# Kernel tuning notes

Hardware: AMD Instinct MI355X
Metric: run time of the kernel (lower is better)

Reference implementation:

```python
import jax, jax.numpy as jnp
import numpy as np

L = 15      # GNN layers
D = 128     # hidden width


def _mlp3(x, w1, b1, w2, b2, w3, b3):
    h = jax.nn.relu(x @ w1 + b1)
    h = jax.nn.relu(h @ w2 + b2)
    return h @ w3 + b3


def _layernorm(x, g, b, eps=1e-5):
    mu = x.mean(-1, keepdims=True)
    var = ((x - mu) ** 2).mean(-1, keepdims=True)
    return (x - mu) / jnp.sqrt(var + eps) * g + b


def _gather(V, idx):
    # V: [B,N,D], idx: [B,E] -> [B,E,D]
    return jax.vmap(lambda v, i: v[i])(V, idx)


def _scatter_sum(e, idx, n):
    # e: [B,E,D], idx: [B,E] -> [B,n,D]
    return jax.vmap(lambda ee, ii: jnp.zeros((n, ee.shape[-1]), ee.dtype).at[ii].add(ee))(e, idx)


def setup_inputs() -> dict:
    key = jax.random.key(0)
    ks = iter(jax.random.split(key, 64))
    B, N, Eg = 1, 10000, 40000

    def lin(fi, fo, pre=()):
        s = 1.0 / np.sqrt(fi)
        w = jax.random.uniform(next(ks), pre + (fi, fo), jnp.float32, -s, s)
        b = jax.random.uniform(next(ks), pre + (fo,), jnp.float32, -s, s)
        return w, b

    inp = {}
    inp['node_pos'] = jax.random.normal(next(ks), (B, N, 3), jnp.float32)
    inp['areas'] = jax.random.uniform(next(ks), (B, N, 1), jnp.float32)
    inp['info'] = jax.random.normal(next(ks), (B, 1, 8), jnp.float32)
    inp['edges'] = jax.random.randint(next(ks), (B, Eg, 2), 0, N, jnp.int32)

    # Encoder MLPs (layer_norm=True)
    for pre, fi in [('fv', 12), ('fe', 4)]:
        w1, b1 = lin(fi, D); w2, b2 = lin(D, D); w3, b3 = lin(D, D)
        inp[pre + '_w1'], inp[pre + '_b1'] = w1, b1
        inp[pre + '_w2'], inp[pre + '_b2'] = w2, b2
        inp[pre + '_w3'], inp[pre + '_b3'] = w3, b3
        inp[pre + '_g'] = jnp.ones((D,), jnp.float32)
        inp[pre + '_bt'] = jnp.zeros((D,), jnp.float32)

    # 15 GNN layers, stacked along leading axis (layer_norm=False)
    for pre, fi in [('ge', D + 2 * D), ('gn', D + D)]:
        w1, b1 = lin(fi, D, (L,)); w2, b2 = lin(D, D, (L,)); w3, b3 = lin(D, D, (L,))
        inp[pre + '_w1'], inp[pre + '_b1'] = w1, b1
        inp[pre + '_w2'], inp[pre + '_b2'] = w2, b2
        inp[pre + '_w3'], inp[pre + '_b3'] = w3, b3

    # Decoder (layer_norm=False, output_size=1)
    w1, b1 = lin(D, D); w2, b2 = lin(D, D); w3, b3 = lin(D, 1)
    inp['de_w1'], inp['de_b1'] = w1, b1
    inp['de_w2'], inp['de_b2'] = w2, b2
    inp['de_w3'], inp['de_b3'] = w3, b3
    return inp


def reference(node_pos, areas, info, edges,
              fv_w1, fv_b1, fv_w2, fv_b2, fv_w3, fv_b3, fv_g, fv_bt,
              fe_w1, fe_b1, fe_w2, fe_b2, fe_w3, fe_b3, fe_g, fe_bt,
              ge_w1, ge_b1, ge_w2, ge_b2, ge_w3, ge_b3,
              gn_w1, gn_b1, gn_w2, gn_b2, gn_w3, gn_b3,
              de_w1, de_b1, de_w2, de_b2, de_w3, de_b3):
    B, N, _ = node_pos.shape
    info_b = jnp.broadcast_to(info, (B, N, info.shape[-1]))
    en_in = jnp.concatenate([node_pos, areas, info_b], -1)  # [B,N,12]

    s, r = edges[..., 0], edges[..., 1]
    dist = _gather(node_pos, s) - _gather(node_pos, r)      # [B,E,3]
    nrm = jnp.sqrt((dist ** 2).sum(-1, keepdims=True))
    E_raw = jnp.concatenate([dist, nrm], -1)                # [B,E,4]

    V = _layernorm(_mlp3(en_in, fv_w1, fv_b1, fv_w2, fv_b2, fv_w3, fv_b3), fv_g, fv_bt)
    E = _layernorm(_mlp3(E_raw, fe_w1, fe_b1, fe_w2, fe_b2, fe_w3, fe_b3), fe_g, fe_bt)

    def step(carry, p):
        V, E = carry
        w1, b1, w2, b2, w3, b3, nw1, nb1, nw2, nb2, nw3, nb3 = p
        e_in = jnp.concatenate([_gather(V, s), _gather(V, r), E], -1)  # [B,E,384]
        e_emb = _mlp3(e_in, w1, b1, w2, b2, w3, b3)
        agg = _scatter_sum(e_emb, s, N)                                # [B,N,128]
        v_emb = _mlp3(jnp.concatenate([V, agg], -1), nw1, nb1, nw2, nb2, nw3, nb3)
        return (V + v_emb, E + e_emb), None

    (V, E), _ = jax.lax.scan(step, (V, E),
                             (ge_w1, ge_b1, ge_w2, ge_b2, ge_w3, ge_b3,
                              gn_w1, gn_b1, gn_w2, gn_b2, gn_w3, gn_b3))

    return _mlp3(V, de_w1, de_b1, de_w2, de_b2, de_w3, de_b3)  # [B,N,1]
```

## Files before the change

kernel.cpp:

```cpp
#include <hip/hip_runtime.h>

#define DD 128
#define N_NODE 10000
#define N_EDGE 40000
#define N_LAYER 15

typedef unsigned short U16;
typedef __attribute__((ext_vector_type(8))) short short8;
typedef __attribute__((ext_vector_type(4))) float f32x4;

enum { A_BF16 = 0, A_EDGE, A_NODE, A_ENCIN, A_ERAW };
enum { EPI_F = 0, EPI_EDGE, EPI_NODE, EPI_DEC };

#define OFF_FV1 0
#define OFF_FV2 4096
#define OFF_FV3 20480
#define OFF_FE1 36864
#define OFF_FE2 40960
#define OFF_FE3 57344
#define OFF_GE1 73728
#define OFF_GE2 811008
#define OFF_GE3 1056768
#define OFF_GN1 1302528
#define OFF_GN2 1794048
#define OFF_GN3 2039808
#define OFF_DE1 2285568
#define OFF_DE2 2301952
#define WT_TOTAL 2318336

static __device__ __forceinline__ U16 f2b(float f) {
    union { float f; unsigned u; } x; x.f = f;
    unsigned u = x.u;
    return (U16)((u + 0x7fffu + ((u >> 16) & 1u)) >> 16);
}
static __device__ __forceinline__ float b2f(U16 u) {
    union { unsigned u; float f; } x; x.u = ((unsigned)u) << 16;
    return x.f;
}

static __device__ __forceinline__ void wgb() {
    __asm__ __volatile__("s_waitcnt lgkmcnt(0)\n\ts_barrier" ::: "memory");
}

struct I4x2 { int4 a, b; };

__global__ __launch_bounds__(256)
void wprep(const float* fv1, const float* fv2, const float* fv3,
           const float* fe1, const float* fe2, const float* fe3,
           const float* ge1, const float* ge2, const float* ge3,
           const float* gn1, const float* gn2, const float* gn3,
           const float* de1, const float* de2, U16* Wt)
{
    int b = blockIdx.x;
    const float* src; U16* dst; int K, Kpad, k0;
    if      (b < 1)   { src = fv1; K = 12;  Kpad = 32;  dst = Wt + OFF_FV1; k0 = b * 32; }
    else if (b < 5)   { src = fv2; K = 128; Kpad = 128; dst = Wt + OFF_FV2; k0 = (b-1)*32; }
    else if (b < 9)   { src = fv3; K = 128; Kpad = 128; dst = Wt + OFF_FV3; k0 = (b-5)*32; }
    else if (b < 10)  { src = fe1; K = 4;   Kpad = 32;  dst = Wt + OFF_FE1; k0 = (b-9)*32; }
    else if (b < 14)  { src = fe2; K = 128; Kpad = 128; dst = Wt + OFF_FE2; k0 = (b-10)*32; }
    else if (b < 18)  { src = fe3; K = 128; Kpad = 128; dst = Wt + OFF_FE3; k0 = (b-14)*32; }
    else if (b < 198) { int r = b-18,  mi = r/12, s = r%12; src = ge1 + (size_t)mi*384*128; K = 384; Kpad = 384; dst = Wt + OFF_GE1 + (size_t)mi*49152; k0 = s*32; }
    else if (b < 258) { int r = b-198, mi = r/4,  s = r%4;  src = ge2 + (size_t)mi*16384;   K = 128; Kpad = 128; dst = Wt + OFF_GE2 + (size_t)mi*16384; k0 = s*32; }
    else if (b < 318) { int r = b-258, mi = r/4,  s = r%4;  src = ge3 + (size_t)mi*16384;   K = 128; Kpad = 128; dst = Wt + OFF_GE3 + (size_t)mi*16384; k0 = s*32; }
    else if (b < 438) { int r = b-318, mi = r/8,  s = r%8;  src = gn1 + (size_t)mi*32768;   K = 256; Kpad = 256; dst = Wt + OFF_GN1 + (size_t)mi*32768; k0 = s*32; }
    else if (b < 498) { int r = b-438, mi = r/4,  s = r%4;  src = gn2 + (size_t)mi*16384;   K = 128; Kpad = 128; dst = Wt + OFF_GN2 + (size_t)mi*16384; k0 = s*32; }
    else if (b < 558) { int r = b-498, mi = r/4,  s = r%4;  src = gn3 + (size_t)mi*16384;   K = 128; Kpad = 128; dst = Wt + OFF_GN3 + (size_t)mi*16384; k0 = s*32; }
    else if (b < 562) { src = de1; K = 128; Kpad = 128; dst = Wt + OFF_DE1; k0 = (b-558)*32; }
    else              { src = de2; K = 128; Kpad = 128; dst = Wt + OFF_DE2; k0 = (b-562)*32; }

    __shared__ float T[32][129];
    #pragma unroll
    for (int i = 0; i < 16; ++i) {
        int l = threadIdx.x + i * 256;
        int kk = l >> 7, n = l & 127;
        int kg = k0 + kk;
        T[kk][n] = (kg < K) ? src[(size_t)kg * 128 + n] : 0.f;
    }
    __syncthreads();
    int n = threadIdx.x >> 1, h = threadIdx.x & 1;
    union { U16 u[16]; int4 v[2]; } o;
    #pragma unroll
    for (int j = 0; j < 16; ++j) o.u[j] = f2b(T[h * 16 + j][n]);
    int4* d = (int4*)(dst + (size_t)n * Kpad + k0 + h * 16);
    d[0] = o.v[0]; d[1] = o.v[1];
}

__global__ __launch_bounds__(256)
void csr_hist(const int* __restrict__ edges, int* __restrict__ cnt, int Eg)
{
    int e = blockIdx.x * 256 + threadIdx.x;
    if (e < Eg) atomicAdd(&cnt[edges[2 * e]], 1);
}

__global__ __launch_bounds__(256)
void csr_scan(const int* __restrict__ cnt, int* __restrict__ rowptr,
              int* __restrict__ cursor, int n)
{
    __shared__ int ps[256];
    int t = threadIdx.x, base = t * 40;
    int s = 0;
    for (int j = 0; j < 40; ++j) if (base + j < n) s += cnt[base + j];
    ps[t] = s; __syncthreads();
    for (int off = 1; off < 256; off <<= 1) {
        int v = (t >= off) ? ps[t - off] : 0;
        __syncthreads();
        ps[t] += v;
        __syncthreads();
    }
    int run = ps[t] - s;
    for (int j = 0; j < 40; ++j) {
        if (base + j < n) {
            rowptr[base + j] = run;
            cursor[base + j] = run;
            run += cnt[base + j];
        }
    }
    if (t == 255) rowptr[n] = ps[255];
}

__global__ __launch_bounds__(256)
void csr_scatter(const int* __restrict__ edges, int* __restrict__ cursor,
                 int* __restrict__ spos, int Eg)
{
    int e = blockIdx.x * 256 + threadIdx.x;
    if (e < Eg) spos[e] = atomicAdd(&cursor[edges[2 * e]], 1);
}

template<int ASRC, int EPI, int K1>
__global__ __launch_bounds__(256)
void mlp3(const U16* __restrict__ Af,
          const U16* __restrict__ W1, const float* __restrict__ b1,
          const U16* __restrict__ W2, const float* __restrict__ b2,
          const U16* __restrict__ W3, const float* __restrict__ b3,
          U16* __restrict__ outh, float* __restrict__ outf,
          const int* __restrict__ edges, const int* __restrict__ rowptr,
          const int* __restrict__ spos, float* __restrict__ eEs,
          const U16* __restrict__ Vh, const U16* __restrict__ Ehp,
          const float* __restrict__ pos, const float* __restrict__ area,
          const float* __restrict__ info, const float* __restrict__ w3f,
          int M)
{
    __shared__ U16 As[2][64][40];
    __shared__ U16 Bs[2][128][40];
    __shared__ U16 Hs[64][132];

    const int tid  = threadIdx.x;
    const int row0 = blockIdx.x * 64;
    const int wave = tid >> 6, lane = tid & 63;
    const int quad = lane >> 4, l16 = lane & 15;
    const int wm = (wave >> 1) * 32;
    const int wn = (wave & 1) * 64;
    const int sr = tid >> 2, sh = tid & 3;
    const int br = tid >> 1, bh = tid & 1;
    const int sm = row0 + sr;
    const bool valid = (sm < M);

    int si = 0, ri = 0, jbeg = 0, jend = 0;
    if ((ASRC == A_EDGE || ASRC == A_ERAW) && valid) {
        si = edges[2 * sm]; ri = edges[2 * sm + 1];
    }
    if (ASRC == A_NODE && valid) { jbeg = rowptr[sm]; jend = rowptr[sm + 1]; }

    f32x4 acc[4][2];

    auto zacc = [&] {
        #pragma unroll
        for (int i = 0; i < 4; ++i)
            #pragma unroll
            for (int j = 0; j < 2; ++j) acc[i][j] = (f32x4)0.f;
    };

    auto ldA = [&](int c) -> int4 {
        if (ASRC == A_ENCIN || ASRC == A_ERAW) {
            union { U16 u[8]; int4 v; } pk;
            #pragma unroll
            for (int j = 0; j < 8; ++j) pk.u[j] = 0;
            if (valid) {
                if (ASRC == A_ENCIN) {
                    #pragma unroll
                    for (int j = 0; j < 8; ++j) {
                        int col = sh * 8 + j;
                        float x = 0.f;
                        if (col < 3)       x = pos[3 * sm + col];
                        else if (col == 3) x = area[sm];
                        else if (col < 12) x = info[col - 4];
                        pk.u[j] = f2b(x);
                    }
                } else if (sh == 0) {
                    float dx = pos[3*si]   - pos[3*ri];
                    float dy = pos[3*si+1] - pos[3*ri+1];
                    float dz = pos[3*si+2] - pos[3*ri+2];
                    float nm = sqrtf(dx*dx + dy*dy + dz*dz);
                    pk.u[0] = f2b(dx); pk.u[1] = f2b(dy);
                    pk.u[2] = f2b(dz); pk.u[3] = f2b(nm);
                }
            }
            return pk.v;
        } else if (ASRC == A_NODE && c >= 4) {
            float a[8];
            #pragma unroll
            for (int i = 0; i < 8; ++i) a[i] = 0.f;
            if (valid) {
                const float* base = eEs + (c - 4) * 32 + sh * 8;
                for (int j = jbeg; j < jend; ++j) {
                    const float4* r = (const float4*)(base + (size_t)j * 128);
                    float4 x0 = r[0], x1 = r[1];
                    a[0]+=x0.x; a[1]+=x0.y; a[2]+=x0.z; a[3]+=x0.w;
                    a[4]+=x1.x; a[5]+=x1.y; a[6]+=x1.z; a[7]+=x1.w;
                }
            }
            union { U16 u[8]; int4 v; } pk;
            #pragma unroll
            for (int i = 0; i < 8; ++i) pk.u[i] = f2b(a[i]);
            return pk.v;
        } else {
            const U16* s;
            if (ASRC == A_BF16)        s = Af + (size_t)sm * K1 + c * 32;
            else if (ASRC == A_EDGE) {
                if (c < 4)             s = Vh  + (size_t)si * 128 + c * 32;
                else if (c < 8)        s = Vh  + (size_t)ri * 128 + (c - 4) * 32;
                else                   s = Ehp + (size_t)sm * 128 + (c - 8) * 32;
            } else                     s = Vh  + (size_t)sm * 128 + c * 32;
            return valid ? *(const int4*)(s + sh * 8) : make_int4(0,0,0,0);
        }
    };

    auto ldW = [&](const U16* W, int Kw, int c) -> I4x2 {
        const U16* s = W + (size_t)br * Kw + c * 32 + bh * 16;
        I4x2 r;
        r.a = ((const int4*)s)[0];
        r.b = ((const int4*)s)[1];
        return r;
    };

    auto wrA = [&](int b, int4 v) { *(int4*)&As[b][sr][sh * 8] = v; };
    auto wrW = [&](int b, I4x2 w) {
        *(int4*)&Bs[b][br][bh * 16]     = w.a;
        *(int4*)&Bs[b][br][bh * 16 + 8] = w.b;
    };

    auto mfA = [&](int b) {
        short8 wf[4], af[2];
        #pragma unroll
        for (int g = 0; g < 4; ++g)
            wf[g] = *(const short8*)&Bs[b][wn + g*16 + l16][quad * 8];
        #pragma unroll
        for (int g = 0; g < 2; ++g)
            af[g] = *(const short8*)&As[b][wm + g*16 + l16][quad * 8];
        #pragma unroll
        for (int wg = 0; wg < 4; ++wg)
            #pragma unroll
            for (int ag = 0; ag < 2; ++ag)
                acc[wg][ag] = __builtin_amdgcn_mfma_f32_16x16x32_bf16(
                    wf[wg], af[ag], acc[wg][ag], 0, 0, 0);
    };

    auto mfH = [&](int c, int b) {
        short8 wf[4], af[2];
        #pragma unroll
        for (int g = 0; g < 4; ++g)
            wf[g] = *(const short8*)&Bs[b][wn + g*16 + l16][quad * 8];
        #pragma unroll
        for (int g = 0; g < 2; ++g)
            af[g] = *(const short8*)&Hs[wm + g*16 + l16][c * 32 + quad * 8];
        #pragma unroll
        for (int wg = 0; wg < 4; ++wg)
            #pragma unroll
            for (int ag = 0; ag < 2; ++ag)
                acc[wg][ag] = __builtin_amdgcn_mfma_f32_16x16x32_bf16(
                    wf[wg], af[ag], acc[wg][ag], 0, 0, 0);
    };

    auto hwrite = [&](const float* bias) {
        #pragma unroll
        for (int wg = 0; wg < 4; ++wg) {
            f32x4 bv = *(const f32x4*)&bias[wn + wg*16 + quad*4];
            #pragma unroll
            for (int ag = 0; ag < 2; ++ag) {
                int m  = wm + ag*16 + l16;
                int n0 = wn + wg*16 + quad*4;
                union { U16 u[4]; uint2 q; } pk;
                #pragma unroll
                for (int rg = 0; rg < 4; ++rg)
                    pk.u[rg] = f2b(fmaxf(acc[wg][ag][rg] + bv[rg], 0.f));
                *(uint2*)&Hs[m][n0] = pk.q;
            }
        }
    };

    int4 ra0, ra1; I4x2 rw0, rw1;
    constexpr int C1 = K1 / 32;

    zacc();
    ra0 = ldA(0); rw0 = ldW(W1, K1, 0);
    if (C1 > 1) { ra1 = ldA(1); rw1 = ldW(W1, K1, 1); }
    wrA(0, ra0); wrW(0, rw0);
    wgb();
    #pragma unroll
    for (int c = 0; c < C1; ++c) {
        if (c + 2 < C1) {
            if ((c & 1) == 0) { ra0 = ldA(c + 2); rw0 = ldW(W1, K1, c + 2); }
            else              { ra1 = ldA(c + 2); rw1 = ldW(W1, K1, c + 2); }
        }
        if (c + 1 < C1) {
            if (((c + 1) & 1) == 0) { wrA(0, ra0); wrW(0, rw0); }
            else                    { wrA(1, ra1); wrW(1, rw1); }
        }
        mfA(c & 1);
        wgb();
    }

    rw0 = ldW(W2, 128, 0); rw1 = ldW(W2, 128, 1);
    hwrite(b1);
    wgb();
    zacc();
    wrW(0, rw0);
    wgb();
    #pragma unroll
    for (int c = 0; c < 4; ++c) {
        if (c + 2 < 4) {
            if ((c & 1) == 0) rw0 = ldW(W2, 128, c + 2);
            else              rw1 = ldW(W2, 128, c + 2);
        }
        if (c + 1 < 4) {
            if (((c + 1) & 1) == 0) wrW(0, rw0);
            else                    wrW(1, rw1);
        }
        mfH(c, c & 1);
        wgb();
    }

    if (EPI == EPI_DEC) {
        hwrite(b2);
        wgb();
        int mg = row0 + sr;
        float v = 0.f;
        if (mg < M) {
            const U16* hr = &Hs[sr][sh * 32];
            const float* wr = w3f + sh * 32;
            #pragma unroll
            for (int j = 0; j < 32; ++j) v += b2f(hr[j]) * wr[j];
        }
        v += __shfl_xor(v, 1);
        v += __shfl_xor(v, 2);
        if (sh == 0 && mg < M) outf[mg] = v + b3[0];
        return;
    }

    rw0 = ldW(W3, 128, 0); rw1 = ldW(W3, 128, 1);
    hwrite(b2);
    wgb();
    zacc();
    wrW(0, rw0);
    wgb();
    #pragma unroll
    for (int c = 0; c < 4; ++c) {
        if (c + 2 < 4) {
            if ((c & 1) == 0) rw0 = ldW(W3, 128, c + 2);
            else              rw1 = ldW(W3, 128, c + 2);
        }
        if (c + 1 < 4) {
            if (((c + 1) & 1) == 0) wrW(0, rw0);
            else                    wrW(1, rw1);
        }
        mfH(c, c & 1);
        wgb();
    }

    f32x4 bvs[4];
    #pragma unroll
    for (int wg = 0; wg < 4; ++wg)
        bvs[wg] = *(const f32x4*)&b3[wn + wg*16 + quad*4];
    #pragma unroll
    for (int ag = 0; ag < 2; ++ag) {
        int mg = row0 + wm + ag*16 + l16;
        if (mg >= M) continue;
        int sp = 0;
        if (EPI == EPI_EDGE) sp = spos[mg];
        #pragma unroll
        for (int wg = 0; wg < 4; ++wg) {
            int n0 = wn + wg*16 + quad*4;
            f32x4 v;
            #pragma unroll
            for (int rg = 0; rg < 4; ++rg) v[rg] = acc[wg][ag][rg] + bvs[wg][rg];
            size_t o = (size_t)mg * 128 + n0;
            if (EPI == EPI_F) {
                *(f32x4*)&outf[o] = v;
            } else {
                f32x4 c = *(f32x4*)&outf[o];
                c += v;
                *(f32x4*)&outf[o] = c;
                union { U16 u[4]; uint2 q; } pk;
                #pragma unroll
                for (int rg = 0; rg < 4; ++rg) pk.u[rg] = f2b(c[rg]);
                *(uint2*)&outh[o] = pk.q;
                if (EPI == EPI_EDGE)
                    *(f32x4*)&eEs[(size_t)sp * 128 + n0] = v;
            }
        }
    }
}

__global__ __launch_bounds__(256)
void ln_kernel(float* __restrict__ X, const float* __restrict__ g,
               const float* __restrict__ b, U16* __restrict__ Xh, int rows)
{
    int row  = blockIdx.x * 4 + (threadIdx.x >> 6);
    int lane = threadIdx.x & 63;
    if (row >= rows) return;
    float x0 = X[row * DD + lane];
    float x1 = X[row * DD + 64 + lane];
    float s = x0 + x1, q = x0 * x0 + x1 * x1;
    #pragma unroll
    for (int off = 32; off; off >>= 1) {
        s += __shfl_xor(s, off);
        q += __shfl_xor(q, off);
    }
    float mu  = s * (1.f / 128.f);
    float var = q * (1.f / 128.f) - mu * mu;
    float inv = rsqrtf(var + 1e-5f);
    float y0 = (x0 - mu) * inv * g[lane]      + b[lane];
    float y1 = (x1 - mu) * inv * g[64 + lane] + b[64 + lane];
    X[row * DD + lane]       = y0;
    X[row * DD + 64 + lane]  = y1;
    Xh[row * DD + lane]      = f2b(y0);
    Xh[row * DD + 64 + lane] = f2b(y1);
}

extern "C" void kernel_launch(void* const* d_in, const int* in_sizes, int n_in,
                              void* d_out, int out_size, void* d_ws, size_t ws_size,
                              hipStream_t stream)
{
    (void)in_sizes; (void)n_in; (void)out_size; (void)ws_size;

    const float* pos   = (const float*)d_in[0];
    const float* area  = (const float*)d_in[1];
    const float* info  = (const float*)d_in[2];
    const int*   edges = (const int*)d_in[3];
    const float* fv_w1 = (const float*)d_in[4];
    const float* fv_b1 = (const float*)d_in[5];
    const float* fv_w2 = (const float*)d_in[6];
    const float* fv_b2 = (const float*)d_in[7];
    const float* fv_w3 = (const float*)d_in[8];
    const float* fv_b3 = (const float*)d_in[9];
    const float* fv_g  = (const float*)d_in[10];
    const float* fv_bt = (const float*)d_in[11];
    const float* fe_w1 = (const float*)d_in[12];
    const float* fe_b1 = (const float*)d_in[13];
    const float* fe_w2 = (const float*)d_in[14];
    const float* fe_b2 = (const float*)d_in[15];
    const float* fe_w3 = (const float*)d_in[16];
    const float* fe_b3 = (const float*)d_in[17];
    const float* fe_g  = (const float*)d_in[18];
    const float* fe_bt = (const float*)d_in[19];
    const float* ge_w1 = (const float*)d_in[20];
    const float* ge_b1 = (const float*)d_in[21];
    const float* ge_w2 = (const float*)d_in[22];
    const float* ge_b2 = (const float*)d_in[23];
    const float* ge_w3 = (const float*)d_in[24];
    const float* ge_b3 = (const float*)d_in[25];
    const float* gn_w1 = (const float*)d_in[26];
    const float* gn_b1 = (const float*)d_in[27];
    const float* gn_w2 = (const float*)d_in[28];
    const float* gn_b2 = (const float*)d_in[29];
    const float* gn_w3 = (const float*)d_in[30];
    const float* gn_b3 = (const float*)d_in[31];
    const float* de_w1 = (const float*)d_in[32];
    const float* de_b1 = (const float*)d_in[33];
    const float* de_w2 = (const float*)d_in[34];
    const float* de_b2 = (const float*)d_in[35];
    const float* de_w3 = (const float*)d_in[36];
    const float* de_b3 = (const float*)d_in[37];

    char* p = (char*)d_ws;
    float* Vf   = (float*)p;  p += (size_t)N_NODE * 128 * 4;
    float* Ef   = (float*)p;  p += (size_t)N_EDGE * 128 * 4;
    float* eEs  = (float*)p;  p += (size_t)N_EDGE * 128 * 4;
    U16*  Vh    = (U16*)p;    p += (size_t)N_NODE * 128 * 2;
    U16*  Eh    = (U16*)p;    p += (size_t)N_EDGE * 128 * 2;
    U16*  Wt    = (U16*)p;    p += (size_t)WT_TOTAL * 2;
    int*  rowptr = (int*)p;   p += (size_t)(N_NODE + 4) * 4;
    int*  cursor = (int*)p;   p += (size_t)N_NODE * 4;
    int*  cnt    = (int*)p;   p += (size_t)N_NODE * 4;
    int*  spos   = (int*)p;   p += (size_t)N_EDGE * 4;

    const int gbE = (N_EDGE + 63) / 64;
    const int gbN = (N_NODE + 63) / 64;

    wprep<<<566, 256, 0, stream>>>(fv_w1, fv_w2, fv_w3, fe_w1, fe_w2, fe_w3,
                                   ge_w1, ge_w2, ge_w3, gn_w1, gn_w2, gn_w3,
                                   de_w1, de_w2, Wt);
    hipMemsetAsync(cnt, 0, (size_t)N_NODE * 4, stream);
    csr_hist<<<(N_EDGE + 255) / 256, 256, 0, stream>>>(edges, cnt, N_EDGE);
    csr_scan<<<1, 256, 0, stream>>>(cnt, rowptr, cursor, N_NODE);
    csr_scatter<<<(N_EDGE + 255) / 256, 256, 0, stream>>>(edges, cursor, spos, N_EDGE);

    mlp3<A_ERAW, EPI_F, 32><<<gbE, 256, 0, stream>>>(
        nullptr, Wt + OFF_FE1, fe_b1, Wt + OFF_FE2, fe_b2, Wt + OFF_FE3, fe_b3,
        nullptr, Ef, edges, nullptr, nullptr, nullptr, nullptr, nullptr,
        pos, nullptr, nullptr, nullptr, N_EDGE);
    ln_kernel<<<(N_EDGE + 3) / 4, 256, 0, stream>>>(Ef, fe_g, fe_bt, Eh, N_EDGE);

    mlp3<A_ENCIN, EPI_F, 32><<<gbN, 256, 0, stream>>>(
        nullptr, Wt + OFF_FV1, fv_b1, Wt + OFF_FV2, fv_b2, Wt + OFF_FV3, fv_b3,
        nullptr, Vf, nullptr, nullptr, nullptr, nullptr, nullptr, nullptr,
        pos, area, info, nullptr, N_NODE);
    ln_kernel<<<(N_NODE + 3) / 4, 256, 0, stream>>>(Vf, fv_g, fv_bt, Vh, N_NODE);

    for (int l = 0; l < N_LAYER; ++l) {
        mlp3<A_EDGE, EPI_EDGE, 384><<<gbE, 256, 0, stream>>>(
            nullptr,
            Wt + OFF_GE1 + (size_t)l * 49152, ge_b1 + (size_t)l * 128,
            Wt + OFF_GE2 + (size_t)l * 16384, ge_b2 + (size_t)l * 128,
            Wt + OFF_GE3 + (size_t)l * 16384, ge_b3 + (size_t)l * 128,
            Eh, Ef, edges, nullptr, spos, eEs, Vh, Eh,
            nullptr, nullptr, nullptr, nullptr, N_EDGE);
        mlp3<A_NODE, EPI_NODE, 256><<<gbN, 256, 0, stream>>>(
            nullptr,
            Wt + OFF_GN1 + (size_t)l * 32768, gn_b1 + (size_t)l * 128,
            Wt + OFF_GN2 + (size_t)l * 16384, gn_b2 + (size_t)l * 128,
            Wt + OFF_GN3 + (size_t)l * 16384, gn_b3 + (size_t)l * 128,
            Vh, Vf, nullptr, rowptr, nullptr, eEs, Vh, nullptr,
            nullptr, nullptr, nullptr, nullptr, N_NODE);
    }

    mlp3<A_BF16, EPI_DEC, 128><<<gbN, 256, 0, stream>>>(
        Vh, Wt + OFF_DE1, de_b1, Wt + OFF_DE2, de_b2, nullptr, de_b3,
        nullptr, (float*)d_out, nullptr, nullptr, nullptr, nullptr, nullptr, nullptr,
        nullptr, nullptr, nullptr, de_w3, N_NODE);
}
```

Before: 1.085 ms.

## Shrink MLP tiles to 32 rows with 128 threads and deepen weight prefetch

The fused three-layer MLP kernel now handles 32 rows per block with two waves, each computing a 32x64 output slice, instead of 64 rows with four waves. This doubles the block count so small node launches fill more CUs. Global-load prefetching goes from two to three register stages, and each thread loads a full 32-wide weight row. It also accumulates neighbour sums in double precision, simplifies the encoder input load, and clamps out-of-range rows rather than branching. The trade-off is that each block reloads the weight tiles for half as many rows, and the FP64 aggregation adds cost.

```diff
diff --git a/kernel.cpp b/kernel.cpp
--- a/kernel.cpp
+++ b/kernel.cpp
@@ -42,7 +42,7 @@
     __asm__ __volatile__("s_waitcnt lgkmcnt(0)\n\ts_barrier" ::: "memory");
 }
 
-struct I4x2 { int4 a, b; };
+struct I4x4 { int4 a, b, c, d; };
 
 __global__ __launch_bounds__(256)
 void wprep(const float* fv1, const float* fv2, const float* fv3,
@@ -127,7 +127,7 @@
 }
 
 template<int ASRC, int EPI, int K1>
-__global__ __launch_bounds__(256)
+__global__ __launch_bounds__(128)
 void mlp3(const U16* __restrict__ Af,
           const U16* __restrict__ W1, const float* __restrict__ b1,
           const U16* __restrict__ W2, const float* __restrict__ b2,
@@ -140,24 +140,23 @@
           const float* __restrict__ info, const float* __restrict__ w3f,
           int M)
 {
-    __shared__ U16 As[2][64][40];
+    __shared__ U16 As[2][32][40];
     __shared__ U16 Bs[2][128][40];
-    __shared__ U16 Hs[64][132];
+    __shared__ U16 Hs[32][136];
 
     const int tid  = threadIdx.x;
-    const int row0 = blockIdx.x * 64;
-    const int wave = tid >> 6, lane = tid & 63;
+    const int row0 = blockIdx.x * 32;
+    const int lane = tid & 63;
     const int quad = lane >> 4, l16 = lane & 15;
-    const int wm = (wave >> 1) * 32;
-    const int wn = (wave & 1) * 64;
+    const int wn = (tid >> 6) * 64;
     const int sr = tid >> 2, sh = tid & 3;
-    const int br = tid >> 1, bh = tid & 1;
     const int sm = row0 + sr;
     const bool valid = (sm < M);
+    const int smc = valid ? sm : 0;
 
     int si = 0, ri = 0, jbeg = 0, jend = 0;
-    if ((ASRC == A_EDGE || ASRC == A_ERAW) && valid) {
-        si = edges[2 * sm]; ri = edges[2 * sm + 1];
+    if (ASRC == A_EDGE || ASRC == A_ERAW) {
+        si = edges[2 * smc]; ri = edges[2 * smc + 1];
     }
     if (ASRC == A_NODE && valid) { jbeg = rowptr[sm]; jend = rowptr[sm + 1]; }
 
@@ -165,9 +164,9 @@
 
     auto zacc = [&] {
         #pragma unroll
-        for (int i = 0; i < 4; ++i)
-            #pragma unroll
-            for (int j = 0; j < 2; ++j) acc[i][j] = (f32x4)0.f;
+        for (int g = 0; g < 4; ++g)
+            #pragma unroll
+            for (int a = 0; a < 2; ++a) acc[g][a] = (f32x4)0.f;
     };
 
     auto ldA = [&](int c) -> int4 {
@@ -177,14 +176,14 @@
             for (int j = 0; j < 8; ++j) pk.u[j] = 0;
             if (valid) {
                 if (ASRC == A_ENCIN) {
-                    #pragma unroll
-                    for (int j = 0; j < 8; ++j) {
-                        int col = sh * 8 + j;
-                        float x = 0.f;
-                        if (col < 3)       x = pos[3 * sm + col];
-                        else if (col == 3) x = area[sm];
-                        else if (col < 12) x = info[col - 4];
-                        pk.u[j] = f2b(x);
+                    if (sh == 0) {
+                        pk.u[0] = f2b(pos[3*sm]); pk.u[1] = f2b(pos[3*sm+1]);
+                        pk.u[2] = f2b(pos[3*sm+2]); pk.u[3] = f2b(area[sm]);
+                        #pragma unroll
+                        for (int j = 0; j < 4; ++j) pk.u[4+j] = f2b(info[j]);
+                    } else if (sh == 1) {
+                        #pragma unroll
+                        for (int j = 0; j < 4; ++j) pk.u[j] = f2b(info[4+j]);
                     }
                 } else if (sh == 0) {
                     float dx = pos[3*si]   - pos[3*ri];
@@ -197,9 +196,9 @@
             }
             return pk.v;
         } else if (ASRC == A_NODE && c >= 4) {
-            float a[8];
-            #pragma unroll
-            for (int i = 0; i < 8; ++i) a[i] = 0.f;
+            double a[8];
+            #pragma unroll
+            for (int i = 0; i < 8; ++i) a[i] = 0.0;
             if (valid) {
                 const float* base = eEs + (c - 4) * 32 + sh * 8;
                 for (int j = jbeg; j < jend; ++j) {
@@ -211,121 +210,107 @@
             }
             union { U16 u[8]; int4 v; } pk;
             #pragma unroll
-            for (int i = 0; i < 8; ++i) pk.u[i] = f2b(a[i]);
+            for (int i = 0; i < 8; ++i) pk.u[i] = f2b((float)a[i]);
             return pk.v;
         } else {
             const U16* s;
-            if (ASRC == A_BF16)        s = Af + (size_t)sm * K1 + c * 32;
+            if (ASRC == A_BF16)        s = Af + (size_t)smc * K1 + c * 32;
             else if (ASRC == A_EDGE) {
                 if (c < 4)             s = Vh  + (size_t)si * 128 + c * 32;
                 else if (c < 8)        s = Vh  + (size_t)ri * 128 + (c - 4) * 32;
-                else                   s = Ehp + (size_t)sm * 128 + (c - 8) * 32;
-            } else                     s = Vh  + (size_t)sm * 128 + c * 32;
-            return valid ? *(const int4*)(s + sh * 8) : make_int4(0,0,0,0);
+                else                   s = Ehp + (size_t)smc * 128 + (c - 8) * 32;
+            } else                     s = Vh  + (size_t)smc * 128 + c * 32;
+            return *(const int4*)(s + sh * 8);
         }
     };
 
-    auto ldW = [&](const U16* W, int Kw, int c) -> I4x2 {
-        const U16* s = W + (size_t)br * Kw + c * 32 + bh * 16;
-        I4x2 r;
-        r.a = ((const int4*)s)[0];
-        r.b = ((const int4*)s)[1];
+    auto ldW = [&](const U16* W, int Kw, int c) -> I4x4 {
+        const int4* s = (const int4*)(W + (size_t)tid * Kw + c * 32);
+        I4x4 r; r.a = s[0]; r.b = s[1]; r.c = s[2]; r.d = s[3];
         return r;
     };
 
     auto wrA = [&](int b, int4 v) { *(int4*)&As[b][sr][sh * 8] = v; };
-    auto wrW = [&](int b, I4x2 w) {
-        *(int4*)&Bs[b][br][bh * 16]     = w.a;
-        *(int4*)&Bs[b][br][bh * 16 + 8] = w.b;
+    auto wrW = [&](int b, I4x4 w) {
+        int4* d = (int4*)&Bs[b][tid][0];
+        d[0] = w.a; d[1] = w.b; d[2] = w.c; d[3] = w.d;
     };
 
     auto mfA = [&](int b) {
         short8 wf[4], af[2];
         #pragma unroll
         for (int g = 0; g < 4; ++g)
-            wf[g] = *(const short8*)&Bs[b][wn + g*16 + l16][quad * 8];
-        #pragma unroll
-        for (int g = 0; g < 2; ++g)
-            af[g] = *(const short8*)&As[b][wm + g*16 + l16][quad * 8];
-        #pragma unroll
-        for (int wg = 0; wg < 4; ++wg)
-            #pragma unroll
-            for (int ag = 0; ag < 2; ++ag)
-                acc[wg][ag] = __builtin_amdgcn_mfma_f32_16x16x32_bf16(
-                    wf[wg], af[ag], acc[wg][ag], 0, 0, 0);
+            wf[g] = *(const short8*)&Bs[b][wn + 16*g + l16][quad * 8];
+        #pragma unroll
+        for (int a = 0; a < 2; ++a)
+            af[a] = *(const short8*)&As[b][16*a + l16][quad * 8];
+        #pragma unroll
+        for (int g = 0; g < 4; ++g)
+            #pragma unroll
+            for (int a = 0; a < 2; ++a)
+                acc[g][a] = __builtin_amdgcn_mfma_f32_16x16x32_bf16(
+                    wf[g], af[a], acc[g][a], 0, 0, 0);
     };
 
     auto mfH = [&](int c, int b) {
         short8 wf[4], af[2];
         #pragma unroll
         for (int g = 0; g < 4; ++g)
-            wf[g] = *(const short8*)&Bs[b][wn + g*16 + l16][quad * 8];
-        #pragma unroll
-        for (int g = 0; g < 2; ++g)
-            af[g] = *(const short8*)&Hs[wm + g*16 + l16][c * 32 + quad * 8];
-        #pragma unroll
-        for (int wg = 0; wg < 4; ++wg)
-            #pragma unroll
-            for (int ag = 0; ag < 2; ++ag)
-                acc[wg][ag] = __builtin_amdgcn_mfma_f32_16x16x32_bf16(
-                    wf[wg], af[ag], acc[wg][ag], 0, 0, 0);
+            wf[g] = *(const short8*)&Bs[b][wn + 16*g + l16][quad * 8];
+        #pragma unroll
+        for (int a = 0; a < 2; ++a)
+            af[a] = *(const short8*)&Hs[16*a + l16][c * 32 + quad * 8];
+        #pragma unroll
+        for (int g = 0; g < 4; ++g)
+            #pragma unroll
+            for (int a = 0; a < 2; ++a)
+                acc[g][a] = __builtin_amdgcn_mfma_f32_16x16x32_bf16(
+                    wf[g], af[a], acc[g][a], 0, 0, 0);
     };
 
     auto hwrite = [&](const float* bias) {
         #pragma unroll
-        for (int wg = 0; wg < 4; ++wg) {
-            f32x4 bv = *(const f32x4*)&bias[wn + wg*16 + quad*4];
-            #pragma unroll
-            for (int ag = 0; ag < 2; ++ag) {
-                int m  = wm + ag*16 + l16;
-                int n0 = wn + wg*16 + quad*4;
+        for (int g = 0; g < 4; ++g) {
+            f32x4 bv = *(const f32x4*)&bias[wn + 16*g + quad*4];
+            #pragma unroll
+            for (int a = 0; a < 2; ++a) {
                 union { U16 u[4]; uint2 q; } pk;
                 #pragma unroll
                 for (int rg = 0; rg < 4; ++rg)
-                    pk.u[rg] = f2b(fmaxf(acc[wg][ag][rg] + bv[rg], 0.f));
-                *(uint2*)&Hs[m][n0] = pk.q;
+                    pk.u[rg] = f2b(fmaxf(acc[g][a][rg] + bv[rg], 0.f));
+                *(uint2*)&Hs[16*a + l16][wn + 16*g + quad*4] = pk.q;
             }
         }
     };
 
-    int4 ra0, ra1; I4x2 rw0, rw1;
+    int4 ra[3]; I4x4 rw[3];
     constexpr int C1 = K1 / 32;
+    constexpr int PD1 = (C1 < 3) ? C1 : 3;
 
     zacc();
-    ra0 = ldA(0); rw0 = ldW(W1, K1, 0);
-    if (C1 > 1) { ra1 = ldA(1); rw1 = ldW(W1, K1, 1); }
-    wrA(0, ra0); wrW(0, rw0);
+    #pragma unroll
+    for (int p = 0; p < PD1; ++p) { ra[p] = ldA(p); rw[p] = ldW(W1, K1, p); }
+    wrA(0, ra[0]); wrW(0, rw[0]);
     wgb();
     #pragma unroll
     for (int c = 0; c < C1; ++c) {
-        if (c + 2 < C1) {
-            if ((c & 1) == 0) { ra0 = ldA(c + 2); rw0 = ldW(W1, K1, c + 2); }
-            else              { ra1 = ldA(c + 2); rw1 = ldW(W1, K1, c + 2); }
-        }
-        if (c + 1 < C1) {
-            if (((c + 1) & 1) == 0) { wrA(0, ra0); wrW(0, rw0); }
-            else                    { wrA(1, ra1); wrW(1, rw1); }
-        }
+        if (c + 3 < C1) { ra[(c+3)%3] = ldA(c+3); rw[(c+3)%3] = ldW(W1, K1, c+3); }
+        if (c + 1 < C1) { wrA((c+1)&1, ra[(c+1)%3]); wrW((c+1)&1, rw[(c+1)%3]); }
         mfA(c & 1);
         wgb();
     }
 
-    rw0 = ldW(W2, 128, 0); rw1 = ldW(W2, 128, 1);
+    #pragma unroll
+    for (int p = 0; p < 3; ++p) rw[p] = ldW(W2, 128, p);
     hwrite(b1);
     wgb();
     zacc();
-    wrW(0, rw0);
+    wrW(0, rw[0]);
     wgb();
     #pragma unroll
     for (int c = 0; c < 4; ++c) {
-        if (c + 2 < 4) {
-            if ((c & 1) == 0) rw0 = ldW(W2, 128, c + 2);
-            else              rw1 = ldW(W2, 128, c + 2);
-        }
-        if (c + 1 < 4) {
-            if (((c + 1) & 1) == 0) wrW(0, rw0);
-            else                    wrW(1, rw1);
-        }
+        if (c + 3 < 4) rw[(c+3)%3] = ldW(W2, 128, c+3);
+        if (c + 1 < 4) wrW((c+1)&1, rw[(c+1)%3]);
         mfH(c, c & 1);
         wgb();
     }
@@ -333,66 +318,61 @@
     if (EPI == EPI_DEC) {
         hwrite(b2);
         wgb();
-        int mg = row0 + sr;
+        int row = tid >> 2, q4 = tid & 3;
+        int mg = row0 + row;
         float v = 0.f;
-        if (mg < M) {
-            const U16* hr = &Hs[sr][sh * 32];
-            const float* wr = w3f + sh * 32;
-            #pragma unroll
-            for (int j = 0; j < 32; ++j) v += b2f(hr[j]) * wr[j];
+        #pragma unroll
+        for (int t = 0; t < 4; ++t) {
+            union { int4 i; U16 u[8]; } x;
+            x.i = *(const int4*)&Hs[row][q4 * 32 + t * 8];
+            const float* wr = w3f + q4 * 32 + t * 8;
+            #pragma unroll
+            for (int j = 0; j < 8; ++j) v += b2f(x.u[j]) * wr[j];
         }
         v += __shfl_xor(v, 1);
         v += __shfl_xor(v, 2);
-        if (sh == 0 && mg < M) outf[mg] = v + b3[0];
+        if (q4 == 0 && mg < M) outf[mg] = v + b3[0];
         return;
     }
 
-    rw0 = ldW(W3, 128, 0); rw1 = ldW(W3, 128, 1);
+    #pragma unroll
+    for (int p = 0; p < 3; ++p) rw[p] = ldW(W3, 128, p);
     hwrite(b2);
     wgb();
     zacc();
-    wrW(0, rw0);
+    wrW(0, rw[0]);
     wgb();
     #pragma unroll
     for (int c = 0; c < 4; ++c) {
-        if (c + 2 < 4) {
-            if ((c & 1) == 0) rw0 = ldW(W3, 128, c + 2);
-            else              rw1 = ldW(W3, 128, c + 2);
-        }
-        if (c + 1 < 4) {
-            if (((c + 1) & 1) == 0) wrW(0, rw0);
-            else                    wrW(1, rw1);
-        }
+        if (c + 3 < 4) rw[(c+3)%3] = ldW(W3, 128, c+3);
+        if (c + 1 < 4) wrW((c+1)&1, rw[(c+1)%3]);
         mfH(c, c & 1);
         wgb();
     }
 
-    f32x4 bvs[4];
-    #pragma unroll
-    for (int wg = 0; wg < 4; ++wg)
-        bvs[wg] = *(const f32x4*)&b3[wn + wg*16 + quad*4];
-    #pragma unroll
-    for (int ag = 0; ag < 2; ++ag) {
-        int mg = row0 + wm + ag*16 + l16;
+    #pragma unroll
+    for (int a = 0; a < 2; ++a) {
+        int mg = row0 + 16*a + l16;
         if (mg >= M) continue;
         int sp = 0;
         if (EPI == EPI_EDGE) sp = spos[mg];
         #pragma unroll
-        for (int wg = 0; wg < 4; ++wg) {
-            int n0 = wn + wg*16 + quad*4;
+        for (int g = 0; g < 4; ++g) {
+            int n0 = wn + 16*g + quad*4;
+            f32x4 bv = *(const f32x4*)&b3[n0];
             f32x4 v;
             #pragma unroll
-            for (int rg = 0; rg < 4; ++rg) v[rg] = acc[wg][ag][rg] + bvs[wg][rg];
+            for (int rg = 0; rg < 4; ++rg) v[rg] = acc[g][a][rg] + bv[rg];
             size_t o = (size_t)mg * 128 + n0;
             if (EPI == EPI_F) {
                 *(f32x4*)&outf[o] = v;
             } else {
-                f32x4 c = *(f32x4*)&outf[o];
-                c += v;
-                *(f32x4*)&outf[o] = c;
+                f32x4 cc = *(f32x4*)&outf[o];
+                cc += v;
+                *(f32x4*)&outf[o] = cc;
                 union { U16 u[4]; uint2 q; } pk;
                 #pragma unroll
-                for (int rg = 0; rg < 4; ++rg) pk.u[rg] = f2b(c[rg]);
+                for (int rg = 0; rg < 4; ++rg) pk.u[rg] = f2b(cc[rg]);
                 *(uint2*)&outh[o] = pk.q;
                 if (EPI == EPI_EDGE)
                     *(f32x4*)&eEs[(size_t)sp * 128 + n0] = v;
@@ -484,8 +464,8 @@
     int*  cnt    = (int*)p;   p += (size_t)N_NODE * 4;
     int*  spos   = (int*)p;   p += (size_t)N_EDGE * 4;
 
-    const int gbE = (N_EDGE + 63) / 64;
-    const int gbN = (N_NODE + 63) / 64;
+    const int gbE = (N_EDGE + 31) / 32;
+    const int gbN = (N_NODE + 31) / 32;
 
     wprep<<<566, 256, 0, stream>>>(fv_w1, fv_w2, fv_w3, fe_w1, fe_w2, fe_w3,
                                    ge_w1, ge_w2, ge_w3, gn_w1, gn_w2, gn_w3,
@@ -495,27 +475,27 @@
     csr_scan<<<1, 256, 0, stream>>>(cnt, rowptr, cursor, N_NODE);
     csr_scatter<<<(N_EDGE + 255) / 256, 256, 0, stream>>>(edges, cursor, spos, N_EDGE);
 
-    mlp3<A_ERAW, EPI_F, 32><<<gbE, 256, 0, stream>>>(
+    mlp3<A_ERAW, EPI_F, 32><<<gbE, 128, 0, stream>>>(
         nullptr, Wt + OFF_FE1, fe_b1, Wt + OFF_FE2, fe_b2, Wt + OFF_FE3, fe_b3,
         nullptr, Ef, edges, nullptr, nullptr, nullptr, nullptr, nullptr,
         pos, nullptr, nullptr, nullptr, N_EDGE);
     ln_kernel<<<(N_EDGE + 3) / 4, 256, 0, stream>>>(Ef, fe_g, fe_bt, Eh, N_EDGE);
 
-    mlp3<A_ENCIN, EPI_F, 32><<<gbN, 256, 0, stream>>>(
+    mlp3<A_ENCIN, EPI_F, 32><<<gbN, 128, 0, stream>>>(
         nullptr, Wt + OFF_FV1, fv_b1, Wt + OFF_FV2, fv_b2, Wt + OFF_FV3, fv_b3,
         nullptr, Vf, nullptr, nullptr, nullptr, nullptr, nullptr, nullptr,
         pos, area, info, nullptr, N_NODE);
     ln_kernel<<<(N_NODE + 3) / 4, 256, 0, stream>>>(Vf, fv_g, fv_bt, Vh, N_NODE);
 
     for (int l = 0; l < N_LAYER; ++l) {
-        mlp3<A_EDGE, EPI_EDGE, 384><<<gbE, 256, 0, stream>>>(
+        mlp3<A_EDGE, EPI_EDGE, 384><<<gbE, 128, 0, stream>>>(
             nullptr,
             Wt + OFF_GE1 + (size_t)l * 49152, ge_b1 + (size_t)l * 128,
             Wt + OFF_GE2 + (size_t)l * 16384, ge_b2 + (size_t)l * 128,
             Wt + OFF_GE3 + (size_t)l * 16384, ge_b3 + (size_t)l * 128,
             Eh, Ef, edges, nullptr, spos, eEs, Vh, Eh,
             nullptr, nullptr, nullptr, nullptr, N_EDGE);
-        mlp3<A_NODE, EPI_NODE, 256><<<gbN, 256, 0, stream>>>(
+        mlp3<A_NODE, EPI_NODE, 256><<<gbN, 128, 0, stream>>>(
             nullptr,
             Wt + OFF_GN1 + (size_t)l * 32768, gn_b1 + (size_t)l * 128,
             Wt + OFF_GN2 + (size_t)l * 16384, gn_b2 + (size_t)l * 128,
@@ -524,7 +504,7 @@
             nullptr, nullptr, nullptr, nullptr, N_NODE);
     }
 
-    mlp3<A_BF16, EPI_DEC, 128><<<gbN, 256, 0, stream>>>(
+    mlp3<A_BF16, EPI_DEC, 128><<<gbN, 128, 0, stream>>>(
         Vh, Wt + OFF_DE1, de_b1, Wt + OFF_DE2, de_b2, nullptr, de_b3,
         nullptr, (float*)d_out, nullptr, nullptr, nullptr, nullptr, nullptr, nullptr,
         nullptr, nullptr, nullptr, de_w3, N_NODE);
```

After: 1.222 ms. 12.6% more time.

## Store edge messages in edge order and gather via CSR index with double accumulation

Applied to the files above, without the earlier changes.

Edge kernel now writes per-edge message rows in natural edge order instead of scattering them into CSR-sorted positions. The CSR build produces an edge index permutation, and the node kernel gathers message rows through it. The aggregation accumulates in double precision. W3 weight prefetch is moved after the hidden write, with a redundant reload. This aims to make edge-kernel stores coalesced and drop the spos lookup, but it adds indirect, non-contiguous reads and FP64 adds in the node aggregation.

```diff
diff --git a/kernel.cpp b/kernel.cpp
--- a/kernel.cpp
+++ b/kernel.cpp
@@ -120,10 +120,10 @@
 
 __global__ __launch_bounds__(256)
 void csr_scatter(const int* __restrict__ edges, int* __restrict__ cursor,
-                 int* __restrict__ spos, int Eg)
+                 int* __restrict__ eidx, int Eg)
 {
     int e = blockIdx.x * 256 + threadIdx.x;
-    if (e < Eg) spos[e] = atomicAdd(&cursor[edges[2 * e]], 1);
+    if (e < Eg) eidx[atomicAdd(&cursor[edges[2 * e]], 1)] = e;
 }
 
 template<int ASRC, int EPI, int K1>
@@ -134,7 +134,7 @@
           const U16* __restrict__ W3, const float* __restrict__ b3,
           U16* __restrict__ outh, float* __restrict__ outf,
           const int* __restrict__ edges, const int* __restrict__ rowptr,
-          const int* __restrict__ spos, float* __restrict__ eEs,
+          const int* __restrict__ eidx, float* __restrict__ eE,
           const U16* __restrict__ Vh, const U16* __restrict__ Ehp,
           const float* __restrict__ pos, const float* __restrict__ area,
           const float* __restrict__ info, const float* __restrict__ w3f,
@@ -197,13 +197,14 @@
             }
             return pk.v;
         } else if (ASRC == A_NODE && c >= 4) {
-            float a[8];
-            #pragma unroll
-            for (int i = 0; i < 8; ++i) a[i] = 0.f;
+            double a[8];
+            #pragma unroll
+            for (int i = 0; i < 8; ++i) a[i] = 0.0;
             if (valid) {
-                const float* base = eEs + (c - 4) * 32 + sh * 8;
+                const float* base = eE + (c - 4) * 32 + sh * 8;
                 for (int j = jbeg; j < jend; ++j) {
-                    const float4* r = (const float4*)(base + (size_t)j * 128);
+                    int e = eidx[j];
+                    const float4* r = (const float4*)(base + (size_t)e * 128);
                     float4 x0 = r[0], x1 = r[1];
                     a[0]+=x0.x; a[1]+=x0.y; a[2]+=x0.z; a[3]+=x0.w;
                     a[4]+=x1.x; a[5]+=x1.y; a[6]+=x1.z; a[7]+=x1.w;
@@ -211,7 +212,7 @@
             }
             union { U16 u[8]; int4 v; } pk;
             #pragma unroll
-            for (int i = 0; i < 8; ++i) pk.u[i] = f2b(a[i]);
+            for (int i = 0; i < 8; ++i) pk.u[i] = f2b((float)a[i]);
             return pk.v;
         } else {
             const U16* s;
@@ -245,8 +246,8 @@
         for (int g = 0; g < 4; ++g)
             wf[g] = *(const short8*)&Bs[b][wn + g*16 + l16][quad * 8];
         #pragma unroll
-        for (int g = 0; g < 2; ++g)
-            af[g] = *(const short8*)&As[b][wm + g*16 + l16][quad * 8];
+        for (int a = 0; a < 2; ++a)
+            af[a] = *(const short8*)&As[b][wm + a*16 + l16][quad * 8];
         #pragma unroll
         for (int wg = 0; wg < 4; ++wg)
             #pragma unroll
@@ -261,8 +262,8 @@
         for (int g = 0; g < 4; ++g)
             wf[g] = *(const short8*)&Bs[b][wn + g*16 + l16][quad * 8];
         #pragma unroll
-        for (int g = 0; g < 2; ++g)
-            af[g] = *(const short8*)&Hs[wm + g*16 + l16][c * 32 + quad * 8];
+        for (int a = 0; a < 2; ++a)
+            af[a] = *(const short8*)&Hs[wm + a*16 + l16][c * 32 + quad * 8];
         #pragma unroll
         for (int wg = 0; wg < 4; ++wg)
             #pragma unroll
@@ -347,11 +348,12 @@
         return;
     }
 
-    rw0 = ldW(W3, 128, 0); rw1 = ldW(W3, 128, 1);
     hwrite(b2);
     wgb();
+
+    rw0 = ldW(W3, 128, 0); rw1 = ldW(W3, 128, 1);
     zacc();
-    wrW(0, rw0);
+    wrW(0, rw0); rw1 = ldW(W3, 128, 1);
     wgb();
     #pragma unroll
     for (int c = 0; c < 4; ++c) {
@@ -375,8 +377,6 @@
     for (int ag = 0; ag < 2; ++ag) {
         int mg = row0 + wm + ag*16 + l16;
         if (mg >= M) continue;
-        int sp = 0;
-        if (EPI == EPI_EDGE) sp = spos[mg];
         #pragma unroll
         for (int wg = 0; wg < 4; ++wg) {
             int n0 = wn + wg*16 + quad*4;
@@ -387,15 +387,15 @@
             if (EPI == EPI_F) {
                 *(f32x4*)&outf[o] = v;
             } else {
-                f32x4 c = *(f32x4*)&outf[o];
-                c += v;
-                *(f32x4*)&outf[o] = c;
+                f32x4 cc = *(f32x4*)&outf[o];
+                cc += v;
+                *(f32x4*)&outf[o] = cc;
                 union { U16 u[4]; uint2 q; } pk;
                 #pragma unroll
-                for (int rg = 0; rg < 4; ++rg) pk.u[rg] = f2b(c[rg]);
+                for (int rg = 0; rg < 4; ++rg) pk.u[rg] = f2b(cc[rg]);
                 *(uint2*)&outh[o] = pk.q;
                 if (EPI == EPI_EDGE)
-                    *(f32x4*)&eEs[(size_t)sp * 128 + n0] = v;
+                    *(f32x4*)&eE[o] = v;
             }
         }
     }
@@ -475,14 +475,14 @@
     char* p = (char*)d_ws;
     float* Vf   = (float*)p;  p += (size_t)N_NODE * 128 * 4;
     float* Ef   = (float*)p;  p += (size_t)N_EDGE * 128 * 4;
-    float* eEs  = (float*)p;  p += (size_t)N_EDGE * 128 * 4;
+    float* eE   = (float*)p;  p += (size_t)N_EDGE * 128 * 4;
     U16*  Vh    = (U16*)p;    p += (size_t)N_NODE * 128 * 2;
     U16*  Eh    = (U16*)p;    p += (size_t)N_EDGE * 128 * 2;
     U16*  Wt    = (U16*)p;    p += (size_t)WT_TOTAL * 2;
     int*  rowptr = (int*)p;   p += (size_t)(N_NODE + 4) * 4;
     int*  cursor = (int*)p;   p += (size_t)N_NODE * 4;
     int*  cnt    = (int*)p;   p += (size_t)N_NODE * 4;
-    int*  spos   = (int*)p;   p += (size_t)N_EDGE * 4;
+    int*  eidx   = (int*)p;   p += (size_t)N_EDGE * 4;
 
     const int gbE = (N_EDGE + 63) / 64;
     const int gbN = (N_NODE + 63) / 64;
@@ -493,7 +493,7 @@
     hipMemsetAsync(cnt, 0, (size_t)N_NODE * 4, stream);
     csr_hist<<<(N_EDGE + 255) / 256, 256, 0, stream>>>(edges, cnt, N_EDGE);
     csr_scan<<<1, 256, 0, stream>>>(cnt, rowptr, cursor, N_NODE);
-    csr_scatter<<<(N_EDGE + 255) / 256, 256, 0, stream>>>(edges, cursor, spos, N_EDGE);
+    csr_scatter<<<(N_EDGE + 255) / 256, 256, 0, stream>>>(edges, cursor, eidx, N_EDGE);
 
     mlp3<A_ERAW, EPI_F, 32><<<gbE, 256, 0, stream>>>(
         nullptr, Wt + OFF_FE1, fe_b1, Wt + OFF_FE2, fe_b2, Wt + OFF_FE3, fe_b3,
@@ -513,14 +513,14 @@
             Wt + OFF_GE1 + (size_t)l * 49152, ge_b1 + (size_t)l * 128,
             Wt + OFF_GE2 + (size_t)l * 16384, ge_b2 + (size_t)l * 128,
             Wt + OFF_GE3 + (size_t)l * 16384, ge_b3 + (size_t)l * 128,
-            Eh, Ef, edges, nullptr, spos, eEs, Vh, Eh,
+            Eh, Ef, edges, nullptr, nullptr, eE, Vh, Eh,
             nullptr, nullptr, nullptr, nullptr, N_EDGE);
         mlp3<A_NODE, EPI_NODE, 256><<<gbN, 256, 0, stream>>>(
             nullptr,
             Wt + OFF_GN1 + (size_t)l * 32768, gn_b1 + (size_t)l * 128,
             Wt + OFF_GN2 + (size_t)l * 16384, gn_b2 + (size_t)l * 128,
             Wt + OFF_GN3 + (size_t)l * 16384, gn_b3 + (size_t)l * 128,
-            Vh, Vf, nullptr, rowptr, nullptr, eEs, Vh, nullptr,
+            Vh, Vf, nullptr, rowptr, eidx, eE, Vh, nullptr,
             nullptr, nullptr, nullptr, nullptr, N_NODE);
     }
 
```

Measured after the change: 1.230 ms. 13.3% more time.
